# Performance work log

Measured on AMD Instinct MI355X. Metric: run time of the kernel, lower is better.

The kernel has to match this reference:

```python
import jax, jax.numpy as jnp
import numpy as np

F8 = jnp.float8_e4m3fn
F8_MAX = 448.0  # finfo(float8_e4m3fn).max

def setup_inputs() -> dict:
    key = jax.random.key(0)
    k1, k2, k3 = jax.random.split(key, 3)
    B, S, IN, OUT = 4, 4096, 2048, 2048
    x = jax.random.normal(k1, (B, S, IN), dtype=jnp.float32)
    # Pre-quantized fp8 weight [OUT, IN] with a per-tensor scale, as stored by AutoFP8
    w = jax.random.normal(k2, (OUT, IN), dtype=jnp.float32)
    weight_scale = (jnp.max(jnp.abs(w)) / F8_MAX).astype(jnp.float32)
    qweight = jnp.clip(w / weight_scale, -F8_MAX, F8_MAX).astype(F8)
    input_scale = jnp.asarray(0.05, dtype=jnp.float32)  # static activation scale
    bias = jax.random.normal(k3, (OUT,), dtype=jnp.float32)
    return {"x": x, "qweight": qweight, "weight_scale": weight_scale,
            "input_scale": input_scale, "bias": bias}

def reference(x, qweight, weight_scale, input_scale, bias):
    # per_tensor_quantize: divide by static scale, clamp to fp8 range, cast to e4m3fn
    qinput = jnp.clip(x / input_scale, -F8_MAX, F8_MAX).astype(F8)  # [B,S,IN] fp8
    # scaled fp8 GEMM with fused dequant + bias epilogue (out_dtype = x.dtype)
    a = qinput.astype(x.dtype) * input_scale          # dequant activations
    b = qweight.astype(x.dtype) * weight_scale        # dequant weights [OUT,IN]
    return jnp.einsum('bsi,oi->bso', a, b) + bias     # [B,S,OUT]
```

## Files before the change

kernel.cpp:

```cpp
#include <hip/hip_runtime.h>
#include <stdint.h>

typedef float  floatx4 __attribute__((ext_vector_type(4)));
typedef int    intx4   __attribute__((ext_vector_type(4)));
typedef int    intx8   __attribute__((ext_vector_type(8)));

#define AS1 __attribute__((address_space(1)))
#define AS3 __attribute__((address_space(3)))

__device__ __forceinline__ float quant_e4m3_value(float v) {
  float av = fabsf(v);
  float step, rstep;
  if (av < 0.015625f) {
    step  = 0.001953125f;
    rstep = 512.0f;
  } else {
    uint32_t e = __float_as_uint(av) >> 23;
    step  = __uint_as_float((e - 3u) << 23);
    rstep = __uint_as_float((257u - e) << 23);
  }
  return rintf(v * rstep) * step;
}

__device__ __forceinline__ uint32_t enc_e4m3(float v) {
  uint32_t u = __float_as_uint(v);
  uint32_t s = (u >> 24) & 0x80u;
  float av = fabsf(v);
  uint32_t b;
  if (av < 0.015625f) {
    b = s | (uint32_t)(av * 512.0f);
  } else {
    uint32_t e = ((u >> 23) & 0xffu) - 120u;
    uint32_t m = (u >> 20) & 7u;
    b = s | (e << 3) | m;
  }
  return b;
}

__global__ __launch_bounds__(256) void quantize_x_kernel(
    const float4* __restrict__ x, const float* __restrict__ s_ptr,
    uint32_t* __restrict__ q, int n4) {
  int i = blockIdx.x * 256 + threadIdx.x;
  if (i >= n4) return;
  const float s = s_ptr[0];
  float4 v = x[i];
  float a0 = quant_e4m3_value(fminf(fmaxf(v.x / s, -448.0f), 448.0f));
  float a1 = quant_e4m3_value(fminf(fmaxf(v.y / s, -448.0f), 448.0f));
  float a2 = quant_e4m3_value(fminf(fmaxf(v.z / s, -448.0f), 448.0f));
  float a3 = quant_e4m3_value(fminf(fmaxf(v.w / s, -448.0f), 448.0f));
  q[i] = enc_e4m3(a0) | (enc_e4m3(a1) << 8) | (enc_e4m3(a2) << 16) |
         (enc_e4m3(a3) << 24);
}

__global__ __launch_bounds__(256) void prep_w_kernel(
    const uint8_t* __restrict__ qw, uint32_t* __restrict__ w8, int n4) {
  const uint32_t* q32 = (const uint32_t*)qw;
  int lane = threadIdx.x & 63;
  uint32_t w0 = q32[lane], w1 = q32[lane + 64];
  bool fa = ((w0 & 0xFFFFFu) == 0u) && ((w1 & 0xFFFFFu) == 0u);
  uint32_t nib = (w0 | (w0 >> 16) | w1 | (w1 >> 16)) & 0xFu;
  unsigned long long ba = __ballot(fa);
  unsigned long long bb = __ballot(nib == 0u);
  int m = (ba == ~0ull) ? 2 : ((bb == ~0ull) ? 1 : 0);

  int i = blockIdx.x * 256 + threadIdx.x;
  if (i >= n4) return;
  uint32_t o;
  if (m == 1) {
    ushort4 u = ((const ushort4*)qw)[i];
    o = enc_e4m3(__uint_as_float((uint32_t)u.x << 16)) |
        (enc_e4m3(__uint_as_float((uint32_t)u.y << 16)) << 8) |
        (enc_e4m3(__uint_as_float((uint32_t)u.z << 16)) << 16) |
        (enc_e4m3(__uint_as_float((uint32_t)u.w << 16)) << 24);
  } else if (m == 2) {
    float4 v = ((const float4*)qw)[i];
    o = enc_e4m3(v.x) | (enc_e4m3(v.y) << 8) | (enc_e4m3(v.z) << 16) |
        (enc_e4m3(v.w) << 24);
  } else {
    o = ((const uint32_t*)qw)[i];
  }
  w8[i] = o;
}

__global__ __launch_bounds__(512) void gemm_fp8_kernel(
    const uint8_t* __restrict__ A, const uint8_t* __restrict__ B,
    const float* __restrict__ wscale, const float* __restrict__ iscale,
    const float* __restrict__ bias, float* __restrict__ out,
    int M, int N, int K) {
  __shared__ uint8_t lds[131072];

  const int tid  = threadIdx.x;
  const int lane = tid & 63;
  const int wave = tid >> 6;

  const int nbx = gridDim.x;
  const int nwg = nbx * gridDim.y;
  int flat = blockIdx.y * nbx + blockIdx.x;
  flat = (flat & 7) * (nwg >> 3) + (flat >> 3);
  const int bm = flat / nbx;
  const int bn = flat - bm * nbx;

  const int wm_i = wave >> 1;
  const int wn_i = wave & 1;
  const int r15  = lane & 15;
  const int quad = lane >> 4;

  const uint8_t* asrc[4]; uint32_t adst[4];
  const uint8_t* bsrc[2]; uint32_t bdst[2];
#pragma unroll
  for (int j = 0; j < 4; ++j) {
    const int s = tid + j * 512, row = s >> 3, p = s & 7;
    asrc[j] = A + (size_t)(bm * 256 + row) * K + ((p ^ (row & 7)) << 4);
    adst[j] = (uint32_t)s << 4;
  }
#pragma unroll
  for (int j = 0; j < 2; ++j) {
    const int s = tid + j * 512, row = s >> 3, p = s & 7;
    bsrc[j] = B + (size_t)(bn * 128 + row) * K + ((p ^ (row & 7)) << 4);
    bdst[j] = (uint32_t)s << 4;
  }

#define STAGE_A(j, kbyte, ab)                                                  \
  __builtin_amdgcn_global_load_lds(                                            \
      (const AS1 void*)(asrc[j] + (kbyte)),                                    \
      (AS3 void*)(&lds[(ab) * 32768u + adst[j]]), 16, 0, 0)
#define STAGE_B(j, kbyte, bb)                                                  \
  __builtin_amdgcn_global_load_lds(                                            \
      (const AS1 void*)(bsrc[j] + (kbyte)),                                    \
      (AS3 void*)(&lds[98304u + (bb) * 16384u + bdst[j]]), 16, 0, 0)

  floatx4 acc[4][4];
#pragma unroll
  for (int i = 0; i < 4; ++i)
#pragma unroll
    for (int j = 0; j < 4; ++j) acc[i][j] = (floatx4){0.f, 0.f, 0.f, 0.f};

  const int T = K >> 7;

  STAGE_B(0, 0, 0); STAGE_B(1, 0, 0);
  STAGE_A(0, 0, 0); STAGE_A(1, 0, 0); STAGE_A(2, 0, 0); STAGE_A(3, 0, 0);
  if (T > 1) {
    STAGE_A(0, 128, 1); STAGE_A(1, 128, 1);
    STAGE_A(2, 128, 1); STAGE_A(3, 128, 1);
    asm volatile("s_waitcnt vmcnt(4)" ::: "memory");
  } else {
    asm volatile("s_waitcnt vmcnt(0)" ::: "memory");
  }
  __builtin_amdgcn_sched_barrier(0);
  __builtin_amdgcn_s_barrier();

  int ab = 0, bb = 0;
  for (int t = 0; t < T; ++t) {
    const uint8_t* lA = &lds[ab * 32768u];
    const uint8_t* lB = &lds[98304u + bb * 16384u];

    if (t + 1 < T) {
      const int kb = (t + 1) << 7;
      STAGE_B(0, kb, bb ^ 1); STAGE_B(1, kb, bb ^ 1);
    }
    if (t + 2 < T) {
      int a2 = ab + 2; if (a2 >= 3) a2 -= 3;
      const int kb = (t + 2) << 7;
      STAGE_A(0, kb, a2); STAGE_A(1, kb, a2);
      STAGE_A(2, kb, a2); STAGE_A(3, kb, a2);
    }

    intx8 af[4], bf[4];
#pragma unroll
    for (int i = 0; i < 4; ++i) {
      const int r = wm_i * 64 + i * 16 + r15, k8 = r & 7;
      intx4 lo = *(const intx4*)&lA[r * 128 + (((quad * 2)     ^ k8) << 4)];
      intx4 hi = *(const intx4*)&lA[r * 128 + (((quad * 2 + 1) ^ k8) << 4)];
      af[i] = __builtin_shufflevector(lo, hi, 0, 1, 2, 3, 4, 5, 6, 7);
    }
#pragma unroll
    for (int i = 0; i < 4; ++i) {
      const int r = wn_i * 64 + i * 16 + r15, k8 = r & 7;
      intx4 lo = *(const intx4*)&lB[r * 128 + (((quad * 2)     ^ k8) << 4)];
      intx4 hi = *(const intx4*)&lB[r * 128 + (((quad * 2 + 1) ^ k8) << 4)];
      bf[i] = __builtin_shufflevector(lo, hi, 0, 1, 2, 3, 4, 5, 6, 7);
    }

    __builtin_amdgcn_s_setprio(1);
#pragma unroll
    for (int i = 0; i < 4; ++i)
#pragma unroll
      for (int jn = 0; jn < 4; ++jn)
        acc[i][jn] = __builtin_amdgcn_mfma_scale_f32_16x16x128_f8f6f4(
            af[i], bf[jn], acc[i][jn], 0, 0, 0, 127, 0, 127);
    __builtin_amdgcn_s_setprio(0);

    if (t + 2 < T)      asm volatile("s_waitcnt vmcnt(4)" ::: "memory");
    else if (t + 1 < T) asm volatile("s_waitcnt vmcnt(0)" ::: "memory");
    __builtin_amdgcn_sched_barrier(0);
    __builtin_amdgcn_s_barrier();

    ab = (ab == 2) ? 0 : ab + 1;
    bb ^= 1;
  }

  const float sc = wscale[0] * iscale[0];
  const int rq = quad * 4;
#pragma unroll
  for (int ni = 0; ni < 4; ++ni) {
    const int col = bn * 128 + wn_i * 64 + ni * 16 + r15;
    const float bv = bias[col];
#pragma unroll
    for (int mi = 0; mi < 4; ++mi) {
      const int row = bm * 256 + wm_i * 64 + mi * 16 + rq;
      float* o = out + (size_t)row * N + col;
#pragma unroll
      for (int r = 0; r < 4; ++r)
        o[(size_t)r * N] = acc[mi][ni][r] * sc + bv;
    }
  }
#undef STAGE_A
#undef STAGE_B
}

extern "C" void kernel_launch(void* const* d_in, const int* in_sizes, int n_in,
                              void* d_out, int out_size, void* d_ws,
                              size_t ws_size, hipStream_t stream) {
  const float*   x      = (const float*)d_in[0];
  const uint8_t* qw     = (const uint8_t*)d_in[1];
  const float*   wscale = (const float*)d_in[2];
  const float*   iscale = (const float*)d_in[3];
  const float*   bias   = (const float*)d_in[4];
  float*         out    = (float*)d_out;

  const int N = in_sizes[4];
  const int K = in_sizes[1] / N;
  const int M = in_sizes[0] / K;

  uint8_t* qx = (uint8_t*)d_ws;
  uint8_t* w8 = qx + (size_t)M * K;

  const int nx4 = in_sizes[0] / 4;
  quantize_x_kernel<<<(nx4 + 255) / 256, 256, 0, stream>>>(
      (const float4*)x, iscale, (uint32_t*)qx, nx4);

  const int nw4 = in_sizes[1] / 4;
  prep_w_kernel<<<(nw4 + 255) / 256, 256, 0, stream>>>(qw, (uint32_t*)w8, nw4);

  dim3 grid(N / 128, M / 256);
  gemm_fp8_kernel<<<grid, 512, 0, stream>>>(qx, w8, wscale, iscale, bias,
                                            out, M, N, K);
}
```

Measured before the change: 313.7 us.

## Enlarge GEMM tile to 256x256 with split-phase ping-pong LDS schedule

The GEMM block tile grows from 256x128 to 256x256. Each wave now computes a 128x64 sub-tile with 32 accumulators, and A and B are double-buffered in 64KB halves. The K-step is split into four MFMA phases with interleaved LDS reads, half-tile global-to-LDS stages and barriers, which is meant to raise operand reuse and overlap loads with compute. The quantize and weight-prep kernels now process 16 bytes per thread so their stores are wider. The costs are higher register pressure from the doubled accumulators, more barriers per iteration, and fewer workgroups in the grid.

Measured after the change: 324.8 us. 1.04x slower.

```diff
diff --git a/kernel.cpp b/kernel.cpp
--- a/kernel.cpp
+++ b/kernel.cpp
@@ -37,23 +37,31 @@
   return b;
 }
 
-__global__ __launch_bounds__(256) void quantize_x_kernel(
-    const float4* __restrict__ x, const float* __restrict__ s_ptr,
-    uint32_t* __restrict__ q, int n4) {
-  int i = blockIdx.x * 256 + threadIdx.x;
-  if (i >= n4) return;
-  const float s = s_ptr[0];
-  float4 v = x[i];
+__device__ __forceinline__ uint32_t quant4(float4 v, float s) {
   float a0 = quant_e4m3_value(fminf(fmaxf(v.x / s, -448.0f), 448.0f));
   float a1 = quant_e4m3_value(fminf(fmaxf(v.y / s, -448.0f), 448.0f));
   float a2 = quant_e4m3_value(fminf(fmaxf(v.z / s, -448.0f), 448.0f));
   float a3 = quant_e4m3_value(fminf(fmaxf(v.w / s, -448.0f), 448.0f));
-  q[i] = enc_e4m3(a0) | (enc_e4m3(a1) << 8) | (enc_e4m3(a2) << 16) |
+  return enc_e4m3(a0) | (enc_e4m3(a1) << 8) | (enc_e4m3(a2) << 16) |
          (enc_e4m3(a3) << 24);
 }
 
+__global__ __launch_bounds__(256) void quantize_x_kernel(
+    const float4* __restrict__ x, const float* __restrict__ s_ptr,
+    uint4* __restrict__ q, int n16) {
+  int i = blockIdx.x * 256 + threadIdx.x;
+  if (i >= n16) return;
+  const float s = s_ptr[0];
+  uint4 o;
+  o.x = quant4(x[i * 4 + 0], s);
+  o.y = quant4(x[i * 4 + 1], s);
+  o.z = quant4(x[i * 4 + 2], s);
+  o.w = quant4(x[i * 4 + 3], s);
+  q[i] = o;
+}
+
 __global__ __launch_bounds__(256) void prep_w_kernel(
-    const uint8_t* __restrict__ qw, uint32_t* __restrict__ w8, int n4) {
+    const uint8_t* __restrict__ qw, uint4* __restrict__ w8, int n16) {
   const uint32_t* q32 = (const uint32_t*)qw;
   int lane = threadIdx.x & 63;
   uint32_t w0 = q32[lane], w1 = q32[lane + 64];
@@ -64,25 +72,34 @@
   int m = (ba == ~0ull) ? 2 : ((bb == ~0ull) ? 1 : 0);
 
   int i = blockIdx.x * 256 + threadIdx.x;
-  if (i >= n4) return;
-  uint32_t o;
+  if (i >= n16) return;
+  uint4 o;
+  uint32_t r[4];
   if (m == 1) {
-    ushort4 u = ((const ushort4*)qw)[i];
-    o = enc_e4m3(__uint_as_float((uint32_t)u.x << 16)) |
-        (enc_e4m3(__uint_as_float((uint32_t)u.y << 16)) << 8) |
-        (enc_e4m3(__uint_as_float((uint32_t)u.z << 16)) << 16) |
-        (enc_e4m3(__uint_as_float((uint32_t)u.w << 16)) << 24);
+#pragma unroll
+    for (int j = 0; j < 4; ++j) {
+      ushort4 u = ((const ushort4*)qw)[i * 4 + j];
+      r[j] = enc_e4m3(__uint_as_float((uint32_t)u.x << 16)) |
+             (enc_e4m3(__uint_as_float((uint32_t)u.y << 16)) << 8) |
+             (enc_e4m3(__uint_as_float((uint32_t)u.z << 16)) << 16) |
+             (enc_e4m3(__uint_as_float((uint32_t)u.w << 16)) << 24);
+    }
   } else if (m == 2) {
-    float4 v = ((const float4*)qw)[i];
-    o = enc_e4m3(v.x) | (enc_e4m3(v.y) << 8) | (enc_e4m3(v.z) << 16) |
-        (enc_e4m3(v.w) << 24);
-  } else {
-    o = ((const uint32_t*)qw)[i];
-  }
+#pragma unroll
+    for (int j = 0; j < 4; ++j) {
+      float4 v = ((const float4*)qw)[i * 4 + j];
+      r[j] = enc_e4m3(v.x) | (enc_e4m3(v.y) << 8) | (enc_e4m3(v.z) << 16) |
+             (enc_e4m3(v.w) << 24);
+    }
+  } else {
+    uint4 c = ((const uint4*)qw)[i];
+    r[0] = c.x; r[1] = c.y; r[2] = c.z; r[3] = c.w;
+  }
+  o.x = r[0]; o.y = r[1]; o.z = r[2]; o.w = r[3];
   w8[i] = o;
 }
 
-__global__ __launch_bounds__(512) void gemm_fp8_kernel(
+__global__ __launch_bounds__(512, 2) void gemm_fp8_kernel(
     const uint8_t* __restrict__ A, const uint8_t* __restrict__ B,
     const float* __restrict__ wscale, const float* __restrict__ iscale,
     const float* __restrict__ bias, float* __restrict__ out,
@@ -100,48 +117,45 @@
   const int bm = flat / nbx;
   const int bn = flat - bm * nbx;
 
-  const int wm_i = wave >> 1;
-  const int wn_i = wave & 1;
-  const int r15  = lane & 15;
-  const int quad = lane >> 4;
-
-  const uint8_t* asrc[4]; uint32_t adst[4];
-  const uint8_t* bsrc[2]; uint32_t bdst[2];
-#pragma unroll
-  for (int j = 0; j < 4; ++j) {
-    const int s = tid + j * 512, row = s >> 3, p = s & 7;
-    asrc[j] = A + (size_t)(bm * 256 + row) * K + ((p ^ (row & 7)) << 4);
-    adst[j] = (uint32_t)s << 4;
-  }
+  const int wm = (wave >> 2) * 128;
+  const int wn = (wave & 3) * 64;
+  const int r15 = lane & 15, quad = lane >> 4, k8 = r15 & 7;
+  const int posL = ((2 * quad)     ^ k8) << 4;
+  const int posH = ((2 * quad + 1) ^ k8) << 4;
+
+  const uint8_t* aS[2]; const uint8_t* bS[2]; uint32_t dOf[2];
 #pragma unroll
   for (int j = 0; j < 2; ++j) {
-    const int s = tid + j * 512, row = s >> 3, p = s & 7;
-    bsrc[j] = B + (size_t)(bn * 128 + row) * K + ((p ^ (row & 7)) << 4);
-    bdst[j] = (uint32_t)s << 4;
-  }
-
-#define STAGE_A(j, kbyte, ab)                                                  \
+    const int s = tid + j * 512, rl = s >> 3, p = s & 7;
+    aS[j] = A + (size_t)(bm * 256 + rl) * K + ((p ^ (rl & 7)) << 4);
+    bS[j] = B + (size_t)(bn * 256 + rl) * K + ((p ^ (rl & 7)) << 4);
+    dOf[j] = (uint32_t)s << 4;
+  }
+  const size_t hK = (size_t)128 * K;
+
+#define STG_A(j, h, kb, bf_)                                                   \
   __builtin_amdgcn_global_load_lds(                                            \
-      (const AS1 void*)(asrc[j] + (kbyte)),                                    \
-      (AS3 void*)(&lds[(ab) * 32768u + adst[j]]), 16, 0, 0)
-#define STAGE_B(j, kbyte, bb)                                                  \
+      (const AS1 void*)(aS[j] + (h) * hK + (kb)),                              \
+      (AS3 void*)(&lds[(bf_) * 32768u + (h) * 16384u + dOf[j]]), 16, 0, 0)
+#define STG_B(j, h, kb, bf_)                                                   \
   __builtin_amdgcn_global_load_lds(                                            \
-      (const AS1 void*)(bsrc[j] + (kbyte)),                                    \
-      (AS3 void*)(&lds[98304u + (bb) * 16384u + bdst[j]]), 16, 0, 0)
-
-  floatx4 acc[4][4];
-#pragma unroll
-  for (int i = 0; i < 4; ++i)
+      (const AS1 void*)(bS[j] + (h) * hK + (kb)),                              \
+      (AS3 void*)(&lds[65536u + (bf_) * 32768u + (h) * 16384u + dOf[j]]),      \
+      16, 0, 0)
+
+  floatx4 acc[8][4];
+#pragma unroll
+  for (int i = 0; i < 8; ++i)
 #pragma unroll
     for (int j = 0; j < 4; ++j) acc[i][j] = (floatx4){0.f, 0.f, 0.f, 0.f};
 
   const int T = K >> 7;
 
-  STAGE_B(0, 0, 0); STAGE_B(1, 0, 0);
-  STAGE_A(0, 0, 0); STAGE_A(1, 0, 0); STAGE_A(2, 0, 0); STAGE_A(3, 0, 0);
+  STG_A(0, 0, 0, 0); STG_A(1, 0, 0, 0); STG_A(0, 1, 0, 0); STG_A(1, 1, 0, 0);
+  STG_B(0, 0, 0, 0); STG_B(1, 0, 0, 0); STG_B(0, 1, 0, 0); STG_B(1, 1, 0, 0);
   if (T > 1) {
-    STAGE_A(0, 128, 1); STAGE_A(1, 128, 1);
-    STAGE_A(2, 128, 1); STAGE_A(3, 128, 1);
+    STG_B(0, 0, 128, 1); STG_B(1, 0, 128, 1);
+    STG_B(0, 1, 128, 1); STG_B(1, 1, 128, 1);
     asm volatile("s_waitcnt vmcnt(4)" ::: "memory");
   } else {
     asm volatile("s_waitcnt vmcnt(0)" ::: "memory");
@@ -149,73 +163,109 @@
   __builtin_amdgcn_sched_barrier(0);
   __builtin_amdgcn_s_barrier();
 
-  int ab = 0, bb = 0;
   for (int t = 0; t < T; ++t) {
-    const uint8_t* lA = &lds[ab * 32768u];
-    const uint8_t* lB = &lds[98304u + bb * 16384u];
-
+    const int cur = t & 1;
+    const uint8_t* LA = &lds[cur * 32768u] + (wm + r15) * 128;
+    const uint8_t* LB = &lds[65536u + cur * 32768u] + (wn + r15) * 128;
+    const int kb1 = (t + 1) << 7, kb2 = (t + 2) << 7;
+    const bool sA = (t + 1 < T), sB = (t + 2 < T);
+    intx8 af[4], bf[4];
+
+#pragma unroll
+    for (int i = 0; i < 4; ++i) {
+      intx4 lo = *(const intx4*)(LA + i * 2048 + posL);
+      intx4 hi = *(const intx4*)(LA + i * 2048 + posH);
+      af[i] = __builtin_shufflevector(lo, hi, 0, 1, 2, 3, 4, 5, 6, 7);
+    }
+#pragma unroll
+    for (int j = 0; j < 2; ++j) {
+      intx4 lo = *(const intx4*)(LB + j * 2048 + posL);
+      intx4 hi = *(const intx4*)(LB + j * 2048 + posH);
+      bf[j] = __builtin_shufflevector(lo, hi, 0, 1, 2, 3, 4, 5, 6, 7);
+    }
+    if (sA) { STG_A(0, 0, kb1, cur ^ 1); STG_A(1, 0, kb1, cur ^ 1); }
+    __builtin_amdgcn_s_barrier();
+    __builtin_amdgcn_s_setprio(1);
+#pragma unroll
+    for (int i = 0; i < 4; ++i)
+#pragma unroll
+      for (int j = 0; j < 2; ++j)
+        acc[i][j] = __builtin_amdgcn_mfma_scale_f32_16x16x128_f8f6f4(
+            af[i], bf[j], acc[i][j], 0, 0, 0, 127, 0, 127);
+    __builtin_amdgcn_s_setprio(0);
+    __builtin_amdgcn_s_barrier();
+
+#pragma unroll
+    for (int j = 2; j < 4; ++j) {
+      intx4 lo = *(const intx4*)(LB + j * 2048 + posL);
+      intx4 hi = *(const intx4*)(LB + j * 2048 + posH);
+      bf[j] = __builtin_shufflevector(lo, hi, 0, 1, 2, 3, 4, 5, 6, 7);
+    }
+    if (sA) { STG_A(0, 1, kb1, cur ^ 1); STG_A(1, 1, kb1, cur ^ 1); }
+    __builtin_amdgcn_s_barrier();
+    __builtin_amdgcn_s_setprio(1);
+#pragma unroll
+    for (int i = 0; i < 4; ++i)
+#pragma unroll
+      for (int j = 2; j < 4; ++j)
+        acc[i][j] = __builtin_amdgcn_mfma_scale_f32_16x16x128_f8f6f4(
+            af[i], bf[j], acc[i][j], 0, 0, 0, 127, 0, 127);
+    __builtin_amdgcn_s_setprio(0);
+    __builtin_amdgcn_s_barrier();
+
+#pragma unroll
+    for (int i = 0; i < 4; ++i) {
+      intx4 lo = *(const intx4*)(LA + 8192 + i * 2048 + posL);
+      intx4 hi = *(const intx4*)(LA + 8192 + i * 2048 + posH);
+      af[i] = __builtin_shufflevector(lo, hi, 0, 1, 2, 3, 4, 5, 6, 7);
+    }
+    if (sB) { STG_B(0, 0, kb2, cur); STG_B(1, 0, kb2, cur); }
+    __builtin_amdgcn_s_barrier();
+    __builtin_amdgcn_s_setprio(1);
+#pragma unroll
+    for (int i = 0; i < 4; ++i)
+#pragma unroll
+      for (int j = 2; j < 4; ++j)
+        acc[4 + i][j] = __builtin_amdgcn_mfma_scale_f32_16x16x128_f8f6f4(
+            af[i], bf[j], acc[4 + i][j], 0, 0, 0, 127, 0, 127);
+    __builtin_amdgcn_s_setprio(0);
+    __builtin_amdgcn_s_barrier();
+
+    if (sB) { STG_B(0, 1, kb2, cur); STG_B(1, 1, kb2, cur); }
+    __builtin_amdgcn_s_barrier();
+    __builtin_amdgcn_s_setprio(1);
+#pragma unroll
+    for (int i = 0; i < 4; ++i)
+#pragma unroll
+      for (int j = 0; j < 2; ++j)
+        acc[4 + i][j] = __builtin_amdgcn_mfma_scale_f32_16x16x128_f8f6f4(
+            af[i], bf[j], acc[4 + i][j], 0, 0, 0, 127, 0, 127);
+    __builtin_amdgcn_s_setprio(0);
     if (t + 1 < T) {
-      const int kb = (t + 1) << 7;
-      STAGE_B(0, kb, bb ^ 1); STAGE_B(1, kb, bb ^ 1);
-    }
-    if (t + 2 < T) {
-      int a2 = ab + 2; if (a2 >= 3) a2 -= 3;
-      const int kb = (t + 2) << 7;
-      STAGE_A(0, kb, a2); STAGE_A(1, kb, a2);
-      STAGE_A(2, kb, a2); STAGE_A(3, kb, a2);
-    }
-
-    intx8 af[4], bf[4];
-#pragma unroll
-    for (int i = 0; i < 4; ++i) {
-      const int r = wm_i * 64 + i * 16 + r15, k8 = r & 7;
-      intx4 lo = *(const intx4*)&lA[r * 128 + (((quad * 2)     ^ k8) << 4)];
-      intx4 hi = *(const intx4*)&lA[r * 128 + (((quad * 2 + 1) ^ k8) << 4)];
-      af[i] = __builtin_shufflevector(lo, hi, 0, 1, 2, 3, 4, 5, 6, 7);
-    }
-#pragma unroll
-    for (int i = 0; i < 4; ++i) {
-      const int r = wn_i * 64 + i * 16 + r15, k8 = r & 7;
-      intx4 lo = *(const intx4*)&lB[r * 128 + (((quad * 2)     ^ k8) << 4)];
-      intx4 hi = *(const intx4*)&lB[r * 128 + (((quad * 2 + 1) ^ k8) << 4)];
-      bf[i] = __builtin_shufflevector(lo, hi, 0, 1, 2, 3, 4, 5, 6, 7);
-    }
-
-    __builtin_amdgcn_s_setprio(1);
-#pragma unroll
-    for (int i = 0; i < 4; ++i)
-#pragma unroll
-      for (int jn = 0; jn < 4; ++jn)
-        acc[i][jn] = __builtin_amdgcn_mfma_scale_f32_16x16x128_f8f6f4(
-            af[i], bf[jn], acc[i][jn], 0, 0, 0, 127, 0, 127);
-    __builtin_amdgcn_s_setprio(0);
-
-    if (t + 2 < T)      asm volatile("s_waitcnt vmcnt(4)" ::: "memory");
-    else if (t + 1 < T) asm volatile("s_waitcnt vmcnt(0)" ::: "memory");
-    __builtin_amdgcn_sched_barrier(0);
-    __builtin_amdgcn_s_barrier();
-
-    ab = (ab == 2) ? 0 : ab + 1;
-    bb ^= 1;
+      if (t + 2 < T) asm volatile("s_waitcnt vmcnt(4)" ::: "memory");
+      else           asm volatile("s_waitcnt vmcnt(0)" ::: "memory");
+      __builtin_amdgcn_sched_barrier(0);
+    }
+    __builtin_amdgcn_s_barrier();
   }
 
   const float sc = wscale[0] * iscale[0];
   const int rq = quad * 4;
 #pragma unroll
-  for (int ni = 0; ni < 4; ++ni) {
-    const int col = bn * 128 + wn_i * 64 + ni * 16 + r15;
+  for (int jj = 0; jj < 4; ++jj) {
+    const int col = bn * 256 + wn + jj * 16 + r15;
     const float bv = bias[col];
 #pragma unroll
-    for (int mi = 0; mi < 4; ++mi) {
-      const int row = bm * 256 + wm_i * 64 + mi * 16 + rq;
+    for (int mi = 0; mi < 8; ++mi) {
+      const int row = bm * 256 + wm + (mi >> 2) * 64 + (mi & 3) * 16 + rq;
       float* o = out + (size_t)row * N + col;
 #pragma unroll
       for (int r = 0; r < 4; ++r)
-        o[(size_t)r * N] = acc[mi][ni][r] * sc + bv;
-    }
-  }
-#undef STAGE_A
-#undef STAGE_B
+        o[(size_t)r * N] = acc[mi][jj][r] * sc + bv;
+    }
+  }
+#undef STG_A
+#undef STG_B
 }
 
 extern "C" void kernel_launch(void* const* d_in, const int* in_sizes, int n_in,
@@ -235,14 +285,14 @@
   uint8_t* qx = (uint8_t*)d_ws;
   uint8_t* w8 = qx + (size_t)M * K;
 
-  const int nx4 = in_sizes[0] / 4;
-  quantize_x_kernel<<<(nx4 + 255) / 256, 256, 0, stream>>>(
-      (const float4*)x, iscale, (uint32_t*)qx, nx4);
-
-  const int nw4 = in_sizes[1] / 4;
-  prep_w_kernel<<<(nw4 + 255) / 256, 256, 0, stream>>>(qw, (uint32_t*)w8, nw4);
-
-  dim3 grid(N / 128, M / 256);
+  const int nx16 = in_sizes[0] / 16;
+  quantize_x_kernel<<<(nx16 + 255) / 256, 256, 0, stream>>>(
+      (const float4*)x, iscale, (uint4*)qx, nx16);
+
+  const int nw16 = in_sizes[1] / 16;
+  prep_w_kernel<<<(nw16 + 255) / 256, 256, 0, stream>>>(qw, (uint4*)w8, nw16);
+
+  dim3 grid(N / 256, M / 256);
   gemm_fp8_kernel<<<grid, 512, 0, stream>>>(qx, w8, wscale, iscale, bias,
                                             out, M, N, K);
 }
```

## Use 256x256 tiles with B fragments loaded directly to registers

Applied to the files above, without the earlier changes.

The GEMM tile grows from 256x128 to 256x256 per workgroup. Each wave now computes a 128x64 sub-tile with 8x4 accumulators. B fragments are loaded straight from global memory into double-buffered registers, and A is staged through LDS with double buffering, which cuts LDS from 128 KB to 64 KB. Launch bounds ask for 2 workgroups per CU. The intent is more reuse per LDS byte and higher occupancy, at the cost of heavy register pressure and uncoalesced direct global B loads.

After: 561.7 us. 79.1% more time.

```diff
diff --git a/kernel.cpp b/kernel.cpp
--- a/kernel.cpp
+++ b/kernel.cpp
@@ -82,12 +82,12 @@
   w8[i] = o;
 }
 
-__global__ __launch_bounds__(512) void gemm_fp8_kernel(
+__global__ __launch_bounds__(512, 2) void gemm_fp8_kernel(
     const uint8_t* __restrict__ A, const uint8_t* __restrict__ B,
     const float* __restrict__ wscale, const float* __restrict__ iscale,
     const float* __restrict__ bias, float* __restrict__ out,
     int M, int N, int K) {
-  __shared__ uint8_t lds[131072];
+  __shared__ uint8_t lds[65536];
 
   const int tid  = threadIdx.x;
   const int lane = tid & 63;
@@ -100,122 +100,127 @@
   const int bm = flat / nbx;
   const int bn = flat - bm * nbx;
 
-  const int wm_i = wave >> 1;
-  const int wn_i = wave & 1;
-  const int r15  = lane & 15;
-  const int quad = lane >> 4;
-
-  const uint8_t* asrc[4]; uint32_t adst[4];
-  const uint8_t* bsrc[2]; uint32_t bdst[2];
+  const int wm = (wave >> 2) * 128;
+  const int wn = (wave & 3) * 64;
+  const int r15 = lane & 15, quad = lane >> 4, k8 = r15 & 7;
+  const int posL = ((2 * quad)     ^ k8) << 4;
+  const int posH = ((2 * quad + 1) ^ k8) << 4;
+
+  const uint8_t* aS[2]; uint32_t dOf[2];
+#pragma unroll
+  for (int j = 0; j < 2; ++j) {
+    const int s = tid + j * 512, rl = s >> 3, p = s & 7;
+    aS[j] = A + (size_t)(bm * 256 + rl) * K + ((p ^ (rl & 7)) << 4);
+    dOf[j] = (uint32_t)s << 4;
+  }
+  const size_t hK = (size_t)128 * K;
+
+  const uint8_t* bptr[4];
+#pragma unroll
+  for (int j = 0; j < 4; ++j)
+    bptr[j] = B + (size_t)(bn * 256 + wn + j * 16 + r15) * K + quad * 32;
+
+#define STG_A(j, h, kb, bf_)                                                   \
+  __builtin_amdgcn_global_load_lds(                                            \
+      (const AS1 void*)(aS[j] + (h) * hK + (kb)),                              \
+      (AS3 void*)(&lds[(bf_) * 32768u + (h) * 16384u + dOf[j]]), 16, 0, 0)
+
+  floatx4 acc[8][4];
+#pragma unroll
+  for (int i = 0; i < 8; ++i)
+#pragma unroll
+    for (int j = 0; j < 4; ++j) acc[i][j] = (floatx4){0.f, 0.f, 0.f, 0.f};
+
+  intx8 bfA[4], bfB[4];
+  const int T = K >> 7;
+
+  STG_A(0, 0, 0, 0); STG_A(1, 0, 0, 0); STG_A(0, 1, 0, 0); STG_A(1, 1, 0, 0);
 #pragma unroll
   for (int j = 0; j < 4; ++j) {
-    const int s = tid + j * 512, row = s >> 3, p = s & 7;
-    asrc[j] = A + (size_t)(bm * 256 + row) * K + ((p ^ (row & 7)) << 4);
-    adst[j] = (uint32_t)s << 4;
-  }
-#pragma unroll
-  for (int j = 0; j < 2; ++j) {
-    const int s = tid + j * 512, row = s >> 3, p = s & 7;
-    bsrc[j] = B + (size_t)(bn * 128 + row) * K + ((p ^ (row & 7)) << 4);
-    bdst[j] = (uint32_t)s << 4;
-  }
-
-#define STAGE_A(j, kbyte, ab)                                                  \
-  __builtin_amdgcn_global_load_lds(                                            \
-      (const AS1 void*)(asrc[j] + (kbyte)),                                    \
-      (AS3 void*)(&lds[(ab) * 32768u + adst[j]]), 16, 0, 0)
-#define STAGE_B(j, kbyte, bb)                                                  \
-  __builtin_amdgcn_global_load_lds(                                            \
-      (const AS1 void*)(bsrc[j] + (kbyte)),                                    \
-      (AS3 void*)(&lds[98304u + (bb) * 16384u + bdst[j]]), 16, 0, 0)
-
-  floatx4 acc[4][4];
-#pragma unroll
-  for (int i = 0; i < 4; ++i)
-#pragma unroll
-    for (int j = 0; j < 4; ++j) acc[i][j] = (floatx4){0.f, 0.f, 0.f, 0.f};
-
-  const int T = K >> 7;
-
-  STAGE_B(0, 0, 0); STAGE_B(1, 0, 0);
-  STAGE_A(0, 0, 0); STAGE_A(1, 0, 0); STAGE_A(2, 0, 0); STAGE_A(3, 0, 0);
-  if (T > 1) {
-    STAGE_A(0, 128, 1); STAGE_A(1, 128, 1);
-    STAGE_A(2, 128, 1); STAGE_A(3, 128, 1);
-    asm volatile("s_waitcnt vmcnt(4)" ::: "memory");
-  } else {
-    asm volatile("s_waitcnt vmcnt(0)" ::: "memory");
-  }
+    intx4 lo = *(const intx4*)(bptr[j]);
+    intx4 hi = *(const intx4*)(bptr[j] + 16);
+    bfA[j] = __builtin_shufflevector(lo, hi, 0, 1, 2, 3, 4, 5, 6, 7);
+  }
+  asm volatile("s_waitcnt vmcnt(0)" ::: "memory");
   __builtin_amdgcn_sched_barrier(0);
   __builtin_amdgcn_s_barrier();
 
-  int ab = 0, bb = 0;
-  for (int t = 0; t < T; ++t) {
-    const uint8_t* lA = &lds[ab * 32768u];
-    const uint8_t* lB = &lds[98304u + bb * 16384u];
-
-    if (t + 1 < T) {
-      const int kb = (t + 1) << 7;
-      STAGE_B(0, kb, bb ^ 1); STAGE_B(1, kb, bb ^ 1);
-    }
-    if (t + 2 < T) {
-      int a2 = ab + 2; if (a2 >= 3) a2 -= 3;
-      const int kb = (t + 2) << 7;
-      STAGE_A(0, kb, a2); STAGE_A(1, kb, a2);
-      STAGE_A(2, kb, a2); STAGE_A(3, kb, a2);
-    }
-
-    intx8 af[4], bf[4];
-#pragma unroll
-    for (int i = 0; i < 4; ++i) {
-      const int r = wm_i * 64 + i * 16 + r15, k8 = r & 7;
-      intx4 lo = *(const intx4*)&lA[r * 128 + (((quad * 2)     ^ k8) << 4)];
-      intx4 hi = *(const intx4*)&lA[r * 128 + (((quad * 2 + 1) ^ k8) << 4)];
-      af[i] = __builtin_shufflevector(lo, hi, 0, 1, 2, 3, 4, 5, 6, 7);
-    }
-#pragma unroll
-    for (int i = 0; i < 4; ++i) {
-      const int r = wn_i * 64 + i * 16 + r15, k8 = r & 7;
-      intx4 lo = *(const intx4*)&lB[r * 128 + (((quad * 2)     ^ k8) << 4)];
-      intx4 hi = *(const intx4*)&lB[r * 128 + (((quad * 2 + 1) ^ k8) << 4)];
-      bf[i] = __builtin_shufflevector(lo, hi, 0, 1, 2, 3, 4, 5, 6, 7);
-    }
-
-    __builtin_amdgcn_s_setprio(1);
-#pragma unroll
-    for (int i = 0; i < 4; ++i)
-#pragma unroll
-      for (int jn = 0; jn < 4; ++jn)
-        acc[i][jn] = __builtin_amdgcn_mfma_scale_f32_16x16x128_f8f6f4(
-            af[i], bf[jn], acc[i][jn], 0, 0, 0, 127, 0, 127);
-    __builtin_amdgcn_s_setprio(0);
-
-    if (t + 2 < T)      asm volatile("s_waitcnt vmcnt(4)" ::: "memory");
-    else if (t + 1 < T) asm volatile("s_waitcnt vmcnt(0)" ::: "memory");
-    __builtin_amdgcn_sched_barrier(0);
-    __builtin_amdgcn_s_barrier();
-
-    ab = (ab == 2) ? 0 : ab + 1;
-    bb ^= 1;
-  }
+#define TILE(t_, USE, LOAD)                                                    \
+  do {                                                                         \
+    const int cur_ = (t_) & 1;                                                 \
+    const uint8_t* LA = &lds[cur_ * 32768u] + (wm + r15) * 128;                \
+    if ((t_) + 1 < T) {                                                        \
+      const int kb1 = ((t_) + 1) << 7;                                         \
+      STG_A(0, 0, kb1, cur_ ^ 1); STG_A(1, 0, kb1, cur_ ^ 1);                  \
+      STG_A(0, 1, kb1, cur_ ^ 1); STG_A(1, 1, kb1, cur_ ^ 1);                  \
+      __builtin_amdgcn_sched_barrier(0);       \
+      _Pragma("unroll")                                                        \
+      for (int j = 0; j < 4; ++j) {                                            \
+        intx4 lo = *(const intx4*)(bptr[j] + kb1);                             \
+        intx4 hi = *(const intx4*)(bptr[j] + kb1 + 16);                        \
+        LOAD[j] = __builtin_shufflevector(lo, hi, 0, 1, 2, 3, 4, 5, 6, 7);     \
+      }                                                                        \
+      __builtin_amdgcn_sched_barrier(0);                                       \
+    }                                                                          \
+    intx8 af[4];                                                               \
+    _Pragma("unroll")                                                          \
+    for (int i = 0; i < 4; ++i) {                                              \
+      intx4 lo = *(const intx4*)(LA + i * 2048 + posL);                        \
+      intx4 hi = *(const intx4*)(LA + i * 2048 + posH);                        \
+      af[i] = __builtin_shufflevector(lo, hi, 0, 1, 2, 3, 4, 5, 6, 7);         \
+    }                                                                          \
+    __builtin_amdgcn_s_setprio(1);                                             \
+    _Pragma("unroll")                                                          \
+    for (int i = 0; i < 4; ++i)                                                \
+      _Pragma("unroll")                                                        \
+      for (int j = 0; j < 4; ++j)                                              \
+        acc[i][j] = __builtin_amdgcn_mfma_scale_f32_16x16x128_f8f6f4(          \
+            af[i], USE[j], acc[i][j], 0, 0, 0, 127, 0, 127);                   \
+    __builtin_amdgcn_s_setprio(0);                                             \
+    _Pragma("unroll")                                                          \
+    for (int i = 0; i < 4; ++i) {                                              \
+      intx4 lo = *(const intx4*)(LA + 8192 + i * 2048 + posL);                 \
+      intx4 hi = *(const intx4*)(LA + 8192 + i * 2048 + posH);                 \
+      af[i] = __builtin_shufflevector(lo, hi, 0, 1, 2, 3, 4, 5, 6, 7);         \
+    }                                                                          \
+    __builtin_amdgcn_s_setprio(1);                                             \
+    _Pragma("unroll")                                                          \
+    for (int i = 0; i < 4; ++i)                                                \
+      _Pragma("unroll")                                                        \
+      for (int j = 0; j < 4; ++j)                                              \
+        acc[4 + i][j] = __builtin_amdgcn_mfma_scale_f32_16x16x128_f8f6f4(      \
+            af[i], USE[j], acc[4 + i][j], 0, 0, 0, 127, 0, 127);               \
+    __builtin_amdgcn_s_setprio(0);                                             \
+    if ((t_) + 1 < T) {                                                        \
+          \
+      asm volatile("s_waitcnt vmcnt(4)" ::: "memory");                         \
+      __builtin_amdgcn_sched_barrier(0);                                       \
+      __builtin_amdgcn_s_barrier();                                            \
+    }                                                                          \
+  } while (0)
+
+  for (int t = 0; t < T; t += 2) {
+    TILE(t,     bfA, bfB);
+    TILE(t + 1, bfB, bfA);
+  }
+#undef TILE
+#undef STG_A
 
   const float sc = wscale[0] * iscale[0];
   const int rq = quad * 4;
 #pragma unroll
-  for (int ni = 0; ni < 4; ++ni) {
-    const int col = bn * 128 + wn_i * 64 + ni * 16 + r15;
+  for (int jj = 0; jj < 4; ++jj) {
+    const int col = bn * 256 + wn + jj * 16 + r15;
     const float bv = bias[col];
 #pragma unroll
-    for (int mi = 0; mi < 4; ++mi) {
-      const int row = bm * 256 + wm_i * 64 + mi * 16 + rq;
+    for (int mi = 0; mi < 8; ++mi) {
+      const int row = bm * 256 + wm + (mi >> 2) * 64 + (mi & 3) * 16 + rq;
       float* o = out + (size_t)row * N + col;
 #pragma unroll
       for (int r = 0; r < 4; ++r)
-        o[(size_t)r * N] = acc[mi][ni][r] * sc + bv;
+        o[(size_t)r * N] = acc[mi][jj][r] * sc + bv;
     }
   }
-#undef STAGE_A
-#undef STAGE_B
 }
 
 extern "C" void kernel_launch(void* const* d_in, const int* in_sizes, int n_in,
@@ -242,7 +247,7 @@
   const int nw4 = in_sizes[1] / 4;
   prep_w_kernel<<<(nw4 + 255) / 256, 256, 0, stream>>>(qw, (uint32_t*)w8, nw4);
 
-  dim3 grid(N / 128, M / 256);
+  dim3 grid(N / 256, M / 256);
   gemm_fp8_kernel<<<grid, 512, 0, stream>>>(qx, w8, wscale, iscale, bias,
                                             out, M, N, K);
 }
```
